# Optimization experiments

Measured on AMD Instinct MI355X. Metric: run time of the kernel, lower is better.

## Reference

```python
import jax, jax.numpy as jnp
import numpy as np

DIM = 96
HEADS = 4
HID = int(DIM * 2.66)  # 255, GDFN hidden width
B, H, W = 4, 128, 128


def _conv(x, w, b=None, groups=1):
    y = jax.lax.conv_general_dilated(x, w, (1, 1), 'SAME',
                                     dimension_numbers=('NCHW', 'OIHW', 'NCHW'),
                                     feature_group_count=groups)
    return y if b is None else y + b[None, :, None, None]


def _ln(x, w, b):
    # WithBias LayerNorm over channel dim (per pixel), biased variance, eps=1e-5
    mu = x.mean(1, keepdims=True)
    var = ((x - mu) ** 2).mean(1, keepdims=True)
    return (x - mu) / jnp.sqrt(var + 1e-5) * w[None, :, None, None] + b[None, :, None, None]


def _l2norm(x):
    # torch F.normalize(dim=-1): x / max(||x||_2, 1e-12)
    return x / jnp.maximum(jnp.linalg.norm(x, axis=-1, keepdims=True), 1e-12)


def _gelu(x):
    return jax.nn.gelu(x, approximate=False)


def setup_inputs() -> dict:
    key = jax.random.key(0)
    ks = iter(jax.random.split(key, 32))
    nrm = lambda shp, s=0.02: jax.random.normal(next(ks), shp, dtype=jnp.float32) * s
    d, h2 = DIM, HID
    inp = {
        'x': jax.random.normal(next(ks), (B, DIM, H, W), dtype=jnp.float32),
        # L_conv: 3x3(d->d,+b) GELU 1x1(d->1,+b)
        'Lc_w1': nrm((d, d, 3, 3)), 'Lc_b1': jnp.zeros((d,), jnp.float32),
        'Lc_w2': nrm((1, d, 1, 1)), 'Lc_b2': jnp.zeros((1,), jnp.float32),
        # R_conv: 3x3(d->d,+b) GELU 1x1(d->3,+b)
        'Rc_w1': nrm((d, d, 3, 3)), 'Rc_b1': jnp.zeros((d,), jnp.float32),
        'Rc_w2': nrm((3, d, 1, 1)), 'Rc_b2': jnp.zeros((3,), jnp.float32),
        # L_rein: 3x3(1->d,+b) GELU ; R_rein: 3x3(3->d,+b)
        'Lr_w': nrm((d, 1, 3, 3)), 'Lr_b': jnp.zeros((d,), jnp.float32),
        'Rr_w': nrm((d, 3, 3, 3)), 'Rr_b': jnp.zeros((d,), jnp.float32),
        # LayerNorms (WithBias)
        'n1_w': jnp.ones((d,), jnp.float32), 'n1_b': jnp.zeros((d,), jnp.float32),
        'nL_w': jnp.ones((d,), jnp.float32), 'nL_b': jnp.zeros((d,), jnp.float32),
        'n2_w': jnp.ones((d,), jnp.float32), 'n2_b': jnp.zeros((d,), jnp.float32),
        # Illum_Attention (bias=False)
        'temp': jnp.ones((HEADS, 1, 1), jnp.float32),
        'q_w': nrm((d, d, 1, 1)),
        'qd_w': nrm((d, d, 3, 3)),          # q_dwconv is a FULL 3x3 conv (no groups)
        'kv_w': nrm((2 * d, d, 1, 1)),
        'kvd_w': nrm((2 * d, 1, 3, 3)),     # depthwise, groups=2*dim
        'po_w': nrm((d, d, 1, 1)),
        # FeedForward (bias=False); NOTE: 'dwconv' here is a FULL 3x3 conv
        'pi_w': nrm((h2, d, 1, 1)),
        'fdw_w': nrm((h2, h2, 3, 3)),
        'fpo_w': nrm((d, h2, 1, 1)),
    }
    return inp


def reference(x, Lc_w1, Lc_b1, Lc_w2, Lc_b2, Rc_w1, Rc_b1, Rc_w2, Rc_b2,
              Lr_w, Lr_b, Rr_w, Rr_b, n1_w, n1_b, nL_w, nL_b, n2_w, n2_b,
              temp, q_w, qd_w, kv_w, kvd_w, po_w, pi_w, fdw_w, fpo_w):
    b, c, h, w = x.shape
    # Retinex decomposition heads
    L = _conv(_gelu(_conv(x, Lc_w1, Lc_b1)), Lc_w2, Lc_b2)   # [b,1,h,w]
    R = _conv(_gelu(_conv(x, Rc_w1, Rc_b1)), Rc_w2, Rc_b2)   # [b,3,h,w]
    L_rein = _gelu(_conv(jax.lax.stop_gradient(L), Lr_w, Lr_b))  # detach in torch
    R_rein = _conv(jax.lax.stop_gradient(R), Rr_w, Rr_b)
    # Illum_Guided_TransformerBlock: x = x + attn(norm1(x), normL(illum))
    xn = _ln(x, n1_w, n1_b)
    ill = _ln(L_rein, nL_w, nL_b)
    q = _conv(_conv(ill, q_w), qd_w)
    kv = _conv(_conv(xn, kv_w), kvd_w, groups=2 * c)
    k, v = jnp.split(kv, 2, axis=1)
    ch, hw = c // HEADS, h * w
    heads = lambda t: t.reshape(b, HEADS, ch, hw)
    qh, kh, vh = _l2norm(heads(q)), _l2norm(heads(k)), heads(v)
    # channel-wise attention: [b,heads,ch,ch]
    attn = jax.nn.softmax(jnp.einsum('bhci,bhdi->bhcd', qh, kh) * temp[None], axis=-1)
    out = jnp.einsum('bhcd,bhdi->bhci', attn, vh).reshape(b, c, h, w)
    x = x + _conv(out, po_w)
    # x = x + ffn(norm2(x))
    x2 = _ln(x, n2_w, n2_b)
    x = x + _conv(_gelu(_conv(_conv(x2, pi_w), fdw_w)), fpo_w)
    x = x + R_rein
    return (x, L, R)
```

## Files before the change

### kernel.cpp

```cpp
#include <hip/hip_runtime.h>

#define HWsz 16384
#define Wd 128

typedef unsigned short ushortT;
typedef unsigned int uintT;
typedef __attribute__((ext_vector_type(8))) short short8v;
typedef __attribute__((ext_vector_type(4))) float f32x4;
typedef __attribute__((ext_vector_type(16))) float f32x16;
typedef __attribute__((ext_vector_type(4))) unsigned short ushort4v;

__device__ __forceinline__ float gelu_f(float x){
    return 0.5f * x * (1.0f + erff(x * 0.70710678118654752f));
}
__device__ __forceinline__ ushortT f2b(float f){
    union { float f; uintT u; } v; v.f = f;
    uintT r = v.u + 0x7FFFu + ((v.u >> 16) & 1u);
    return (ushortT)(r >> 16);
}
__device__ __forceinline__ float b2f(ushortT u){
    union { uintT u; float f; } v; v.u = ((uintT)u) << 16; return v.f;
}
__device__ __forceinline__ void gload_lds16(const ushortT* g, ushortT* l){
    __builtin_amdgcn_global_load_lds(
        (const __attribute__((address_space(1))) void*)g,
        (__attribute__((address_space(3))) void*)l, 16, 0, 0);
}

__device__ __forceinline__ void pack3_one(int e, const float* __restrict__ w,
    ushortT* __restrict__ outp, int cout, int cin, int BN, int NCH)
{
    int j = e & 7; int r = e >> 3;
    int ocl = r % BN; r /= BN;
    int kg  = r & 3;  r >>= 2;
    int tap = r % 9;  r /= 9;
    int ch  = r % NCH;
    int nt  = r / NCH;
    int ci = ch*32 + kg*8 + j;
    int oc = nt*BN + ocl;
    float v = (oc < cout && ci < cin) ? w[((size_t)oc*cin + ci)*9 + tap] : 0.f;
    outp[e] = f2b(v);
}
__device__ __forceinline__ void pack1_one(int e, const float* __restrict__ w,
    ushortT* __restrict__ outp, int cout, int cin, int BN, int NCH)
{
    int j = e & 7; int r = e >> 3;
    int ocl = r % BN; r /= BN;
    int kg  = r & 3;  r >>= 2;
    int ch  = r % NCH;
    int nt  = r / NCH;
    int ci = ch*32 + kg*8 + j;
    int oc = nt*BN + ocl;
    float v = (oc < cout && ci < cin) ? w[(size_t)oc*cin + ci] : 0.f;
    outp[e] = f2b(v);
}
__global__ __launch_bounds__(256) void pack_all_kernel(
    const float* Lc, const float* Rc, const float* Qd, const float* Fd,
    const float* Q1, const float* KV1, const float* PI1, const float* FPO1,
    ushortT* dL, ushortT* dR, ushortT* dQ, ushortT* dF,
    ushortT* dq0, ushortT* dkv, ushortT* dpi, ushortT* dfpo)
{
    int e = blockIdx.x*256 + threadIdx.x;
    if      (e < 82944)  pack3_one(e,        Lc, dL, 96, 96, 48, 3);
    else if (e < 165888) pack3_one(e-82944,  Rc, dR, 96, 96, 48, 3);
    else if (e < 248832) pack3_one(e-165888, Qd, dQ, 96, 96, 48, 3);
    else if (e < 912384) pack3_one(e-248832, Fd, dF, 255,255, 48, 8);
    else if (e < 921600) pack1_one(e-912384, Q1, dq0, 96, 96, 96, 3);
    else if (e < 940032) pack1_one(e-921600, KV1,dkv, 192,96, 48, 3);
    else if (e < 964608) pack1_one(e-940032, PI1,dpi, 255,96, 64, 3);
    else if (e < 989184) pack1_one(e-964608, FPO1,dfpo,96,255, 96, 8);
}

__global__ __launch_bounds__(256) void tonhwc_ln_kernel(
    const float* __restrict__ in, const float* __restrict__ w,
    const float* __restrict__ bias, ushortT* __restrict__ xh,
    ushortT* __restrict__ xnh)
{
    const int p = blockIdx.x*256 + threadIdx.x;
    const int b = blockIdx.y;
    const float* ip = in + (size_t)b*96*HWsz + p;
    float v[96]; float s=0.f;
#pragma unroll
    for(int c=0;c<96;c++){ v[c]=ip[(size_t)c*HWsz]; s+=v[c]; }
    const float mu = s*(1.f/96.f);
    float s2=0.f;
#pragma unroll
    for(int c=0;c<96;c++){ float d=v[c]-mu; s2+=d*d; }
    const float inv = 1.f/sqrtf(s2*(1.f/96.f)+1e-5f);
    ushortT* op1 = xh  + ((size_t)b*HWsz + p)*96;
    ushortT* op2 = xnh + ((size_t)b*HWsz + p)*96;
#pragma unroll
    for (int g=0; g<12; g++){
        uint4 pk1, pk2; uintT a4[4], n4[4];
#pragma unroll
        for (int i=0;i<4;i++){
            float x0 = v[g*8+2*i], x1v = v[g*8+2*i+1];
            a4[i] = (uintT)f2b(x0) | ((uintT)f2b(x1v)<<16);
            float r0 = (x0-mu)*inv*w[g*8+2*i]+bias[g*8+2*i];
            float r1 = (x1v-mu)*inv*w[g*8+2*i+1]+bias[g*8+2*i+1];
            n4[i] = (uintT)f2b(r0) | ((uintT)f2b(r1)<<16);
        }
        pk1.x=a4[0]; pk1.y=a4[1]; pk1.z=a4[2]; pk1.w=a4[3];
        pk2.x=n4[0]; pk2.y=n4[1]; pk2.z=n4[2]; pk2.w=n4[3];
        *(uint4*)(op1 + g*8) = pk1;
        *(uint4*)(op2 + g*8) = pk2;
    }
}

template<int NG, int NCH, int ACT, int TWOOUT, int OMODE>
__global__ __launch_bounds__(256,3) void conv3x3_v4(
    const ushortT* __restrict__ inh,
    const ushortT* __restrict__ wpk1, const ushortT* __restrict__ wpk2,
    const float* __restrict__ bias1, const float* __restrict__ bias2,
    ushortT* __restrict__ out1, ushortT* __restrict__ out2,
    int cout, int ocpad)
{
    constexpr int BN = NG*16;
    constexpr int Cpad = NCH*32;
    constexpr int WCH4 = 9*4*BN;
    constexpr int WI = (WCH4 + 255)/256;
    __shared__ __align__(16) ushortT As[4*324*8];
    __shared__ __align__(16) ushortT Ws[WCH4*8];

    const int tid = threadIdx.x;
    const int l   = tid & 63;
    const int wv  = tid >> 6;
    const int l15 = l & 15;
    const int kg  = l >> 4;
    const int tix = blockIdx.x & 7, tiy = blockIdx.x >> 3;
    const int b   = blockIdx.z;
    const int x0 = tix*16, y0 = tiy*16;

    int nt = blockIdx.y;
    const ushortT* wpk; const float* bias; ushortT* outp; int ntw;
    if (TWOOUT && nt >= 2){ wpk = wpk2; bias = bias2; outp = out2; ntw = nt-2; }
    else { wpk = wpk1; bias = bias1; outp = out1; ntw = nt; }
    const int ocbase = ntw*BN;

    f32x4 acc[4][NG];
#pragma unroll
    for (int m=0;m<4;m++)
#pragma unroll
        for (int n=0;n<NG;n++) acc[m][n] = (f32x4){0.f,0.f,0.f,0.f};

    const ushortT* inb = inh + (size_t)b*HWsz*Cpad;

    for (int ch=0; ch<NCH; ch++){
        __syncthreads();
        for (int t=tid; t<1296; t+=256){
            int p = t>>2, g = t&3;
            int hy = p/18, hx = p - hy*18;
            int gy = y0 + hy - 1, gx = x0 + hx - 1;
            uint4 v; v.x=0u; v.y=0u; v.z=0u; v.w=0u;
            if ((unsigned)gy < 128u && (unsigned)gx < 128u)
                v = *(const uint4*)(inb + (size_t)(gy*Wd+gx)*Cpad + ch*32 + g*8);
            *(uint4*)(As + (g*324+p)*8) = v;
        }
        {
            const ushortT* wsrc = wpk + ((size_t)ntw*NCH + ch)*(WCH4*8);
#pragma unroll
            for (int i=0; i<WI; i++){
                int t = i*256 + tid;
                if ((WCH4 & 255) == 0 || t < WCH4)
                    gload_lds16(wsrc + (size_t)t*8, Ws + (size_t)t*8);
            }
        }
        __syncthreads();
#pragma unroll
        for (int tp=0; tp<9; tp++){
            const int dy = tp/3, dx = tp - dy*3;
            short8v bf[NG];
#pragma unroll
            for (int n=0;n<NG;n++)
                bf[n] = *(const short8v*)(Ws + ((size_t)(tp*4 + kg)*BN + n*16 + l15)*8);
#pragma unroll
            for (int mg=0;mg<4;mg++){
                short8v a = *(const short8v*)(As + (kg*324 + (wv*4+mg+dy)*18 + l15+dx)*8);
#pragma unroll
                for (int n=0;n<NG;n++)
                    acc[mg][n] = __builtin_amdgcn_mfma_f32_16x16x32_bf16(a, bf[n], acc[mg][n], 0,0,0);
            }
        }
    }
    if (OMODE == 1){
        __syncthreads();
        ushortT* Ts = As + wv*1024;
#pragma unroll
        for (int mg=0;mg<4;mg++){
            int gy = y0 + wv*4 + mg;
            ushortT* orow = outp + ((size_t)b*HWsz + gy*Wd + x0)*ocpad + ocbase;
#pragma unroll
            for (int n=0;n<NG;n++){
                int ocl = n*16 + l15;
                int oc  = ocbase + ocl;
                float bs = (bias && oc < cout) ? bias[oc] : 0.f;
#pragma unroll
                for (int j=0;j<4;j++){
                    int pxj = kg*4 + j;
                    float r = 0.f;
                    if (oc < cout){ r = acc[mg][n][j] + bs; if (ACT) r = gelu_f(r); }
                    int seg = ((ocl>>3) + pxj) & 7;
                    Ts[pxj*64 + seg*8 + (ocl&7)] = f2b(r);
                }
            }
#pragma unroll
            for (int ps=0; ps < (BN+31)/32; ps++){
                int rpx = l & 15;
                int rs  = (l>>4) + ps*4;
                if (rs*8 < BN && ocbase + rs*8 + 8 <= ocpad){
                    int pseg = (rs + rpx) & 7;
                    short8v v = *(const short8v*)(Ts + rpx*64 + pseg*8);
                    *(short8v*)(orow + (size_t)rpx*ocpad + rs*8) = v;
                }
            }
        }
    } else {
#pragma unroll
        for (int n=0;n<NG;n++){
            int oc = ocbase + n*16 + l15;
            if (oc < cout){
                float bs = bias ? bias[oc] : 0.f;
#pragma unroll
                for (int mg=0;mg<4;mg++){
                    int gy = y0 + wv*4 + mg;
                    int gx = x0 + kg*4;
                    ushort4v pk;
#pragma unroll
                    for (int j=0;j<4;j++){
                        float r = acc[mg][n][j] + bs;
                        if (ACT) r = gelu_f(r);
                        pk[j] = f2b(r);
                    }
                    *(ushort4v*)(outp + ((size_t)b*cout + oc)*HWsz + gy*Wd + gx) = pk;
                }
            }
        }
    }
}

template<int NGW, int NCH>
__global__ __launch_bounds__(256) void gemm1x1_v2(
    const ushortT* __restrict__ inh, const ushortT* __restrict__ wpk,
    ushortT* __restrict__ outp, int cout, int ocpad)
{
    constexpr int BN = NGW*16;
    constexpr int Cpad = NCH*32;
    __shared__ __align__(16) ushortT Ts[4*16*64];

    const int tid = threadIdx.x;
    const int l = tid & 63, wv = tid >> 6, l15 = l & 15, kg = l >> 4;
    const int p0 = blockIdx.x*64;
    const int b  = blockIdx.z;
    const int nt = wv, ocbase = wv*BN;
    const ushortT* inb = inh + (size_t)b*HWsz*Cpad;

    f32x4 acc[4][NGW];
#pragma unroll
    for (int m=0;m<4;m++)
#pragma unroll
        for (int n=0;n<NGW;n++) acc[m][n] = (f32x4){0.f,0.f,0.f,0.f};

#pragma unroll
    for (int ch=0; ch<NCH; ch++){
        short8v a[4], bw[NGW];
#pragma unroll
        for (int mg=0; mg<4; mg++)
            a[mg] = *(const short8v*)(inb + (size_t)(p0 + mg*16 + l15)*Cpad + ch*32 + kg*8);
#pragma unroll
        for (int n=0;n<NGW;n++)
            bw[n] = *(const short8v*)(wpk + (((size_t)(nt*NCH + ch)*4 + kg)*BN + n*16 + l15)*8);
#pragma unroll
        for (int mg=0;mg<4;mg++)
#pragma unroll
            for (int n=0;n<NGW;n++)
                acc[mg][n] = __builtin_amdgcn_mfma_f32_16x16x32_bf16(a[mg], bw[n], acc[mg][n], 0,0,0);
    }
    ushortT* Tw = Ts + wv*1024;
#pragma unroll
    for (int mg=0;mg<4;mg++){
        ushortT* orow = outp + ((size_t)b*HWsz + p0 + mg*16)*ocpad + ocbase;
#pragma unroll
        for (int n=0;n<NGW;n++){
            int ocl = n*16 + l15;
            int oc  = ocbase + ocl;
#pragma unroll
            for (int j=0;j<4;j++){
                int pxj = kg*4 + j;
                float r = (oc < cout) ? acc[mg][n][j] : 0.f;
                int seg = ((ocl>>3) + pxj) & 7;
                Tw[pxj*64 + seg*8 + (ocl&7)] = f2b(r);
            }
        }
#pragma unroll
        for (int ps=0; ps < (BN+31)/32; ps++){
            int rpx = l & 15;
            int rs  = (l>>4) + ps*4;
            if (rs*8 < BN){
                int pseg = (rs + rpx) & 7;
                short8v v = *(const short8v*)(Tw + rpx*64 + pseg*8);
                *(short8v*)(orow + (size_t)rpx*ocpad + rs*8) = v;
            }
        }
    }
}

template<int NG, int NCH, int RES, int OMODE, int XMAP>
__global__ __launch_bounds__(256) void gemm1x1_mfma(
    const ushortT* __restrict__ inh, const ushortT* __restrict__ wpk, int wstride_z,
    const float* __restrict__ res1, const ushortT* __restrict__ res2b,
    void* __restrict__ outv, int cout, int ocpad)
{
    constexpr int BN = NG*16;
    constexpr int Cpad = NCH*32;
    constexpr int LSTR = (BN <= 64) ? 64 : 128;
    constexpr int MASK = LSTR/8 - 1;
    __shared__ __align__(16) ushortT TsS[(OMODE==1) ? 4*16*LSTR : 16];

    const int tid = threadIdx.x;
    const int l = tid & 63, wv = tid >> 6, l15 = l & 15, kg = l >> 4;
    int chunk = blockIdx.x, nt = blockIdx.y, b = blockIdx.z;
    const int p0 = chunk*256 + wv*64;
    const ushortT* inb = inh + (size_t)b*HWsz*Cpad;
    const ushortT* wp  = wpk + (size_t)b*wstride_z;

    f32x4 acc[4][NG];
#pragma unroll
    for (int m=0;m<4;m++)
#pragma unroll
        for (int n=0;n<NG;n++) acc[m][n] = (f32x4){0.f,0.f,0.f,0.f};

#pragma unroll
    for (int ch=0; ch<NCH; ch++){
        short8v a[4], bw[NG];
#pragma unroll
        for (int mg=0; mg<4; mg++)
            a[mg] = *(const short8v*)(inb + (size_t)(p0 + mg*16 + l15)*Cpad + ch*32 + kg*8);
#pragma unroll
        for (int n=0;n<NG;n++)
            bw[n] = *(const short8v*)(wp + (((size_t)(nt*NCH + ch)*4 + kg)*BN + n*16 + l15)*8);
#pragma unroll
        for (int mg=0;mg<4;mg++)
#pragma unroll
            for (int n=0;n<NG;n++)
                acc[mg][n] = __builtin_amdgcn_mfma_f32_16x16x32_bf16(a[mg], bw[n], acc[mg][n], 0,0,0);
    }
    if (OMODE == 0){
        float* out = (float*)outv;
#pragma unroll
        for (int n=0;n<NG;n++){
            int oc = nt*BN + n*16 + l15;
            if (oc < cout){
#pragma unroll
                for (int mg=0;mg<4;mg++){
                    int pix = p0 + mg*16 + kg*4;
                    size_t idx = ((size_t)b*cout + oc)*HWsz + pix;
                    float4 r;
                    r.x = acc[mg][n][0]; r.y = acc[mg][n][1];
                    r.z = acc[mg][n][2]; r.w = acc[mg][n][3];
                    if (RES>=1){ float4 q = *(const float4*)(res1+idx); r.x+=q.x;r.y+=q.y;r.z+=q.z;r.w+=q.w; }
                    if (RES>=2){
                        ushort4v q = *(const ushort4v*)(res2b+idx);
                        r.x+=b2f(q[0]); r.y+=b2f(q[1]); r.z+=b2f(q[2]); r.w+=b2f(q[3]);
                    }
                    *(float4*)(out + idx) = r;
                }
            }
        }
    } else {
        ushortT* outp = (ushortT*)outv;
        ushortT* Ts = TsS + wv*(16*LSTR);
#pragma unroll
        for (int mg=0;mg<4;mg++){
            ushortT* orow = outp + ((size_t)b*HWsz + p0 + mg*16)*ocpad + nt*BN;
#pragma unroll
            for (int n=0;n<NG;n++){
                int ocl = n*16 + l15;
                int oc  = nt*BN + ocl;
#pragma unroll
                for (int j=0;j<4;j++){
                    int pxj = kg*4 + j;
                    float r = (oc < cout) ? acc[mg][n][j] : 0.f;
                    int seg = ((ocl>>3) + pxj) & MASK;
                    Ts[pxj*LSTR + seg*8 + (ocl&7)] = f2b(r);
                }
            }
#pragma unroll
            for (int ps=0; ps < (BN+31)/32; ps++){
                int rpx = l & 15;
                int rs  = (l>>4) + ps*4;
                if (rs*8 < BN){
                    int pseg = (rs + rpx) & MASK;
                    short8v v = *(const short8v*)(Ts + rpx*LSTR + pseg*8);
                    *(short8v*)(orow + (size_t)rpx*ocpad + rs*8) = v;
                }
            }
        }
    }
}

__global__ __launch_bounds__(256) void pvpo_ln_kernel(
    const ushortT* __restrict__ vh, const ushortT* __restrict__ Mpk,
    const float* __restrict__ xres, const float* __restrict__ lnw,
    const float* __restrict__ lnb, float* __restrict__ x1out,
    ushortT* __restrict__ x2nh)
{
    constexpr int BN = 96, NG = 6, NCH = 3, Cpad = 96, LSTR = 128, MASK = 15;
    __shared__ __align__(16) ushortT TsS[4*16*LSTR];

    const int tid = threadIdx.x;
    const int l = tid & 63, wv = tid >> 6, l15 = l & 15, kg = l >> 4;
    const int b = blockIdx.z;
    const int p0 = blockIdx.x*256 + wv*64;
    const ushortT* inb = vh + (size_t)b*HWsz*Cpad;
    const ushortT* wp  = Mpk + (size_t)b*9216;

    f32x4 acc[4][NG];
#pragma unroll
    for (int m=0;m<4;m++)
#pragma unroll
        for (int n=0;n<NG;n++) acc[m][n] = (f32x4){0.f,0.f,0.f,0.f};

#pragma unroll
    for (int ch=0; ch<NCH; ch++){
        short8v a[4], bw[NG];
#pragma unroll
        for (int mg=0; mg<4; mg++)
            a[mg] = *(const short8v*)(inb + (size_t)(p0 + mg*16 + l15)*Cpad + ch*32 + kg*8);
#pragma unroll
        for (int n=0;n<NG;n++)
            bw[n] = *(const short8v*)(wp + (((size_t)ch*4 + kg)*BN + n*16 + l15)*8);
#pragma unroll
        for (int mg=0;mg<4;mg++)
#pragma unroll
            for (int n=0;n<NG;n++)
                acc[mg][n] = __builtin_amdgcn_mfma_f32_16x16x32_bf16(a[mg], bw[n], acc[mg][n], 0,0,0);
    }
#pragma unroll
    for (int mg=0;mg<4;mg++){
#pragma unroll
        for (int n=0;n<NG;n++){
            int oc = n*16 + l15;
            int pix = p0 + mg*16 + kg*4;
            size_t idx = ((size_t)b*96 + oc)*HWsz + pix;
            float4 q = *(const float4*)(xres+idx);
            acc[mg][n][0] += q.x; acc[mg][n][1] += q.y;
            acc[mg][n][2] += q.z; acc[mg][n][3] += q.w;
            float4 r;
            r.x = acc[mg][n][0]; r.y = acc[mg][n][1];
            r.z = acc[mg][n][2]; r.w = acc[mg][n][3];
            *(float4*)(x1out + idx) = r;
        }
    }
    float nv[4][NG][4];
#pragma unroll
    for (int mg=0;mg<4;mg++){
#pragma unroll
        for (int j=0;j<4;j++){
            float s = 0.f;
#pragma unroll
            for (int n=0;n<NG;n++) s += acc[mg][n][j];
#pragma unroll
            for (int m=1; m<16; m<<=1) s += __shfl_xor(s, m, 64);
            float mu = s*(1.f/96.f);
            float s2 = 0.f;
#pragma unroll
            for (int n=0;n<NG;n++){ float d = acc[mg][n][j]-mu; s2 += d*d; }
#pragma unroll
            for (int m=1; m<16; m<<=1) s2 += __shfl_xor(s2, m, 64);
            float inv = 1.f/sqrtf(s2*(1.f/96.f) + 1e-5f);
#pragma unroll
            for (int n=0;n<NG;n++){
                int oc = n*16 + l15;
                nv[mg][n][j] = (acc[mg][n][j]-mu)*inv*lnw[oc]+lnb[oc];
            }
        }
    }
    ushortT* Ts = TsS + wv*(16*LSTR);
#pragma unroll
    for (int mg=0;mg<4;mg++){
        ushortT* orow = x2nh + ((size_t)b*HWsz + p0 + mg*16)*96;
#pragma unroll
        for (int n=0;n<NG;n++){
            int ocl = n*16 + l15;
#pragma unroll
            for (int j=0;j<4;j++){
                int pxj = kg*4 + j;
                int seg = ((ocl>>3) + pxj) & MASK;
                Ts[pxj*LSTR + seg*8 + (ocl&7)] = f2b(nv[mg][n][j]);
            }
        }
#pragma unroll
        for (int ps=0; ps<3; ps++){
            int rpx = l & 15;
            int rs  = (l>>4) + ps*4;
            int pseg = (rs + rpx) & MASK;
            short8v v = *(const short8v*)(Ts + rpx*LSTR + pseg*8);
            *(short8v*)(orow + (size_t)rpx*96 + rs*8) = v;
        }
    }
}

template<int NOUT>
__global__ __launch_bounds__(256) void head1x1_kernel(
    const ushortT* __restrict__ inh, const float* __restrict__ w,
    const float* __restrict__ bias, float* __restrict__ out)
{
    __shared__ float lw[NOUT*96];
    const int tid = threadIdx.x;
    for (int t=tid; t<NOUT*96; t+=256) lw[t] = w[t];
    __syncthreads();
    const int p = blockIdx.x*256 + tid;
    const int b = blockIdx.y;
    const ushortT* ip = inh + ((size_t)b*HWsz + p)*96;
    float v[96];
#pragma unroll
    for (int g=0; g<12; g++){
        short8v s = *(const short8v*)(ip + g*8);
#pragma unroll
        for (int i=0;i<8;i++) v[g*8+i] = b2f((ushortT)s[i]);
    }
#pragma unroll
    for (int oc=0; oc<NOUT; oc++){
        float acc = bias[oc];
#pragma unroll
        for (int c=0;c<96;c++) acc += v[c]*lw[oc*96+c];
        out[((size_t)b*NOUT + oc)*HWsz + p] = acc;
    }
}

__global__ __launch_bounds__(256) void lrein_ln_kernel(
    const float* __restrict__ L, const float* __restrict__ w,
    const float* __restrict__ bias, const float* __restrict__ lnw,
    const float* __restrict__ lnb, ushortT* __restrict__ outh)
{
    __shared__ float sw[864], sb[96], sn1[96], sn2[96];
    const int tid = threadIdx.x;
    for (int t=tid; t<864; t+=256) sw[t] = w[t];
    if (tid < 96){ sb[tid]=bias[tid]; sn1[tid]=lnw[tid]; sn2[tid]=lnb[tid]; }
    __syncthreads();
    const int p = blockIdx.x*256 + tid;
    const int b = blockIdx.y;
    const int y = p>>7, x = p&127;
    const float* ib = L + (size_t)b*HWsz;
    float win[9];
#pragma unroll
    for (int dy=0;dy<3;dy++)
#pragma unroll
        for (int dx=0;dx<3;dx++){
            int gy=y+dy-1, gx=x+dx-1;
            win[dy*3+dx] = ((unsigned)gy<128u && (unsigned)gx<128u) ? ib[gy*Wd+gx] : 0.f;
        }
    float v[96]; float s=0.f;
#pragma unroll
    for (int c=0;c<96;c++){
        float a = sb[c];
#pragma unroll
        for (int t=0;t<9;t++) a += win[t]*sw[c*9+t];
        a = gelu_f(a);
        v[c]=a; s+=a;
    }
    const float mu = s*(1.f/96.f);
    float s2=0.f;
#pragma unroll
    for (int c=0;c<96;c++){ float d=v[c]-mu; s2+=d*d; }
    const float inv = 1.f/sqrtf(s2*(1.f/96.f)+1e-5f);
    ushortT* op = outh + ((size_t)b*HWsz + p)*96;
#pragma unroll
    for (int g=0; g<12; g++){
        uint4 pk; uintT w4[4];
#pragma unroll
        for (int i=0;i<4;i++){
            float r0 = (v[g*8+2*i]-mu)*inv*sn1[g*8+2*i]+sn2[g*8+2*i];
            float r1 = (v[g*8+2*i+1]-mu)*inv*sn1[g*8+2*i+1]+sn2[g*8+2*i+1];
            w4[i] = (uintT)f2b(r0) | ((uintT)f2b(r1)<<16);
        }
        pk.x=w4[0]; pk.y=w4[1]; pk.z=w4[2]; pk.w=w4[3];
        *(uint4*)(op + g*8) = pk;
    }
}

__global__ __launch_bounds__(256) void conv3x3_rr_kernel(
    const float* __restrict__ in, const float* __restrict__ w,
    const float* __restrict__ bias, ushortT* __restrict__ out)
{
    __shared__ float sw[216], sb[8];
    const int oc0 = blockIdx.y*8;
    if (threadIdx.x < 216) sw[threadIdx.x] = w[(size_t)oc0*27 + threadIdx.x];
    if (threadIdx.x < 8)   sb[threadIdx.x] = bias[oc0 + threadIdx.x];
    __syncthreads();
    const int p = blockIdx.x*256+threadIdx.x;
    const int b = blockIdx.z;
    const int y=p>>7, x=p&127;
    const float* ib = in + (size_t)b*3*HWsz;
    float win[27];
#pragma unroll
    for (int ci=0;ci<3;ci++)
#pragma unroll
        for (int dy=0;dy<3;dy++)
#pragma unroll
            for (int dx=0;dx<3;dx++){
                int gy=y+dy-1, gx=x+dx-1;
                win[ci*9+dy*3+dx] = ((unsigned)gy<128u && (unsigned)gx<128u)
                    ? ib[(size_t)ci*HWsz + gy*Wd+gx] : 0.f;
            }
#pragma unroll
    for (int i=0;i<8;i++){
        float acc = sb[i];
#pragma unroll
        for (int t=0;t<27;t++) acc += win[t]*sw[i*27+t];
        out[((size_t)b*96 + oc0+i)*HWsz + p] = f2b(acc);
    }
}

__global__ __launch_bounds__(256) void dw_nhwc_kernel(
    const ushortT* __restrict__ inh, const float* __restrict__ w,
    ushortT* __restrict__ kout, ushortT* __restrict__ vouth)
{
    const int p = blockIdx.x*256+threadIdx.x;
    const int c0 = blockIdx.y*8;
    const int b = blockIdx.z;
    const int y=p>>7, x=p&127;
    float lw[72];
#pragma unroll
    for (int i=0;i<8;i++)
#pragma unroll
        for (int t=0;t<9;t++) lw[i*9+t] = w[(size_t)(c0+i)*9 + t];
    const ushortT* ib = inh + (size_t)b*HWsz*192;
    float acc[8];
#pragma unroll
    for (int i=0;i<8;i++) acc[i]=0.f;
#pragma unroll
    for(int dy=0;dy<3;dy++){
        int gy=y+dy-1;
        if((unsigned)gy<128u){
#pragma unroll
            for(int dx=0;dx<3;dx++){
                int gx=x+dx-1;
                if((unsigned)gx<128u){
                    short8v s = *(const short8v*)(ib + (size_t)(gy*Wd+gx)*192 + c0);
#pragma unroll
                    for (int i=0;i<8;i++) acc[i] += b2f((ushortT)s[i])*lw[i*9+dy*3+dx];
                }
            }
        }
    }
    if (c0 < 96){
#pragma unroll
        for (int i=0;i<8;i++)
            kout[((size_t)b*96 + c0+i)*HWsz + p] = f2b(acc[i]);
    } else {
        ushortT* op = vouth + ((size_t)b*HWsz + p)*96 + (c0-96);
        uint4 pk;
        pk.x = (uintT)f2b(acc[0]) | ((uintT)f2b(acc[1])<<16);
        pk.y = (uintT)f2b(acc[2]) | ((uintT)f2b(acc[3])<<16);
        pk.z = (uintT)f2b(acc[4]) | ((uintT)f2b(acc[5])<<16);
        pk.w = (uintT)f2b(acc[6]) | ((uintT)f2b(acc[7])<<16);
        *(uint4*)op = pk;
    }
}

__global__ __launch_bounds__(256) void rownorm_bf16_kernel(
    const ushortT* __restrict__ qb, const ushortT* __restrict__ kb,
    float* __restrict__ invqk)
{
    __shared__ float red[256];
    const int r = blockIdx.x;
    const ushortT* ip = (r < 384) ? (qb + (size_t)r*HWsz) : (kb + (size_t)(r-384)*HWsz);
    float s=0.f;
    const ushortT* tp = ip + threadIdx.x*64;
#pragma unroll
    for (int g=0; g<8; g++){
        short8v v = *(const short8v*)(tp + g*8);
#pragma unroll
        for (int i=0;i<8;i++){ float f = b2f((ushortT)v[i]); s += f*f; }
    }
    red[threadIdx.x]=s; __syncthreads();
    for(int st=128; st>0; st>>=1){
        if(threadIdx.x<st) red[threadIdx.x]+=red[threadIdx.x+st];
        __syncthreads();
    }
    if(threadIdx.x==0) invqk[r] = 1.f/fmaxf(sqrtf(red[0]), 1e-12f);
}

__global__ __launch_bounds__(256) void qk_mfma_kernel(
    const ushortT* __restrict__ qb, const ushortT* __restrict__ kb,
    float* __restrict__ part)
{
    const int tid = threadIdx.x;
    const int l = tid & 63, wv = tid >> 6;
    const int chunk = blockIdx.x*4 + wv;
    const int bh = blockIdx.y, b = bh>>2, h = bh&3;
    const int ch = min(l & 31, 23);
    const int kh = (l >> 5)*8;
    const ushortT* qp = qb + ((size_t)b*96 + h*24 + ch)*HWsz + chunk*512 + kh;
    const ushortT* kp = kb + ((size_t)b*96 + h*24 + ch)*HWsz + chunk*512 + kh;
    f32x16 acc;
#pragma unroll
    for (int r=0;r<16;r++) acc[r]=0.f;
    for (int ks=0; ks<32; ks++){
        short8v a  = *(const short8v*)(qp + ks*16);
        short8v bb = *(const short8v*)(kp + ks*16);
        acc = __builtin_amdgcn_mfma_f32_32x32x16_bf16(a, bb, acc, 0,0,0);
    }
    float* op = part + ((size_t)chunk*16 + bh)*1024;
    const int col = l & 31;
#pragma unroll
    for (int r=0;r<16;r++){
        int row = (r&3) + 8*(r>>2) + 4*(l>>5);
        op[row*32 + col] = acc[r];
    }
}

__global__ __launch_bounds__(576) void softmax_kernel(
    const float* __restrict__ part, const float* __restrict__ invq,
    const float* __restrict__ invk, const float* __restrict__ temp,
    float* __restrict__ attn)
{
    __shared__ float l[576];
    const int bh=blockIdx.x, b=bh>>2, h=bh&3;
    const int tid=threadIdx.x;
    const int i=tid/24, j=tid-i*24;
    float s=0.f;
    for (int c=0;c<32;c++) s += part[((size_t)c*16 + bh)*1024 + i*32 + j];
    l[tid] = s * invq[b*96+h*24+i] * invk[b*96+h*24+j] * temp[h];
    __syncthreads();
    if(tid<24){
        float m=-1e30f;
#pragma unroll
        for(int jj=0;jj<24;jj++) m = fmaxf(m, l[tid*24+jj]);
        float e[24]; float sm=0.f;
#pragma unroll
        for(int jj=0;jj<24;jj++){ e[jj]=__expf(l[tid*24+jj]-m); sm+=e[jj]; }
        float isv = 1.f/sm;
#pragma unroll
        for(int jj=0;jj<24;jj++) attn[(size_t)bh*576 + tid*24 + jj] = e[jj]*isv;
    }
}

__global__ __launch_bounds__(256) void mkM_kernel(
    const float* __restrict__ attn, const float* __restrict__ po_w,
    ushortT* __restrict__ Mpk)
{
    const int b = blockIdx.x;
    for (int e = threadIdx.x; e < 9216; e += 256){
        int oc = e / 96, d = e - oc*96;
        int h = d / 24, dl = d - h*24;
        const float* aw = attn + ((size_t)(b*4+h))*576 + dl;
        const float* pw = po_w + (size_t)oc*96 + h*24;
        float s = 0.f;
#pragma unroll
        for (int c=0;c<24;c++) s += pw[c]*aw[c*24];
        int ch = d>>5, kg = (d>>3)&3, j = d&7;
        Mpk[(size_t)b*9216 + ((size_t)(ch*4+kg)*96 + oc)*8 + j] = f2b(s);
    }
}

extern "C" void kernel_launch(void* const* d_in, const int* in_sizes, int n_in,
                              void* d_out, int out_size, void* d_ws, size_t ws_size,
                              hipStream_t stream)
{
    const float* x     = (const float*)d_in[0];
    const float* Lc_w1 = (const float*)d_in[1];
    const float* Lc_b1 = (const float*)d_in[2];
    const float* Lc_w2 = (const float*)d_in[3];
    const float* Lc_b2 = (const float*)d_in[4];
    const float* Rc_w1 = (const float*)d_in[5];
    const float* Rc_b1 = (const float*)d_in[6];
    const float* Rc_w2 = (const float*)d_in[7];
    const float* Rc_b2 = (const float*)d_in[8];
    const float* Lr_w  = (const float*)d_in[9];
    const float* Lr_b  = (const float*)d_in[10];
    const float* Rr_w  = (const float*)d_in[11];
    const float* Rr_b  = (const float*)d_in[12];
    const float* n1_w  = (const float*)d_in[13];
    const float* n1_b  = (const float*)d_in[14];
    const float* nL_w  = (const float*)d_in[15];
    const float* nL_b  = (const float*)d_in[16];
    const float* n2_w  = (const float*)d_in[17];
    const float* n2_b  = (const float*)d_in[18];
    const float* temp  = (const float*)d_in[19];
    const float* q_w   = (const float*)d_in[20];
    const float* qd_w  = (const float*)d_in[21];
    const float* kv_w  = (const float*)d_in[22];
    const float* kvd_w = (const float*)d_in[23];
    const float* po_w  = (const float*)d_in[24];
    const float* pi_w  = (const float*)d_in[25];
    const float* fdw_w = (const float*)d_in[26];
    const float* fpo_w = (const float*)d_in[27];

    char* base = (char*)d_ws;
    ushortT* xh   = (ushortT*)(base + 0);
    ushortT* f0h  = (ushortT*)(base + 0);
    ushortT* Lh   = (ushortT*)(base + 33554432);
    ushortT* kv0h = (ushortT*)(base + 33554432);
    ushortT* f1h  = (ushortT*)(base + 33554432);
    ushortT* Rh   = (ushortT*)(base + 67108864);
    ushortT* vh   = (ushortT*)(base + 67108864);
    ushortT* x2nh = (ushortT*)(base + 67108864);
    ushortT* illh = (ushortT*)(base + 79691776);
    ushortT* xnh  = (ushortT*)(base + 92274688);
    ushortT* q0h  = (ushortT*)(base + 104857600);
    ushortT* qb   = (ushortT*)(base + 117440512);
    float*   x1   = (float*)(base + 117440512);
    ushortT* kb   = (ushortT*)(base + 142606336);
    ushortT* Bb   = (ushortT*)(base + 155189248);
    char* smb = base + 167772160;
    ushortT* wpkL = (ushortT*)smb;   smb += 165888;
    ushortT* wpkR = (ushortT*)smb;   smb += 165888;
    ushortT* wpkQ = (ushortT*)smb;   smb += 165888;
    ushortT* wpkF = (ushortT*)smb;   smb += 1327104;
    ushortT* wq0  = (ushortT*)smb;   smb += 18432;
    ushortT* wkv  = (ushortT*)smb;   smb += 36864;
    ushortT* wpi  = (ushortT*)smb;   smb += 49152;
    ushortT* wfpo = (ushortT*)smb;   smb += 49152;
    ushortT* Mpk  = (ushortT*)smb;   smb += 73728;
    float* invqk  = (float*)smb;     smb += 3072;
    float* part   = (float*)smb;     smb += 2097152;
    float* attn   = (float*)smb;     smb += 36864;

    float* out_x = (float*)d_out;
    float* out_L = out_x + (size_t)4*96*HWsz;
    float* out_R = out_L + (size_t)4*HWsz;

    dim3 blk(256);

    hipLaunchKernelGGL(pack_all_kernel, dim3(3864), blk, 0, stream,
        Lc_w1, Rc_w1, qd_w, fdw_w, q_w, kv_w, pi_w, fpo_w,
        wpkL, wpkR, wpkQ, wpkF, wq0, wkv, wpi, wfpo);
    hipLaunchKernelGGL(tonhwc_ln_kernel, dim3(64,4), blk, 0, stream, x, n1_w, n1_b, xh, xnh);

    hipLaunchKernelGGL((conv3x3_v4<3,3,1,1,1>), dim3(64,4,4), blk, 0, stream,
        xh, wpkL, wpkR, Lc_b1, Rc_b1, Lh, Rh, 96, 96);
    hipLaunchKernelGGL((head1x1_kernel<1>), dim3(64,4), blk, 0, stream, Lh, Lc_w2, Lc_b2, out_L);
    hipLaunchKernelGGL((head1x1_kernel<3>), dim3(64,4), blk, 0, stream, Rh, Rc_w2, Rc_b2, out_R);
    hipLaunchKernelGGL(lrein_ln_kernel, dim3(64,4), blk, 0, stream, out_L, Lr_w, Lr_b, nL_w, nL_b, illh);
    hipLaunchKernelGGL(conv3x3_rr_kernel, dim3(64,12,4), blk, 0, stream, out_R, Rr_w, Rr_b, Bb);

    hipLaunchKernelGGL((gemm1x1_mfma<6,3,0,1,0>), dim3(64,1,4), blk, 0, stream,
        illh, wq0, 0, nullptr, nullptr, (void*)q0h, 96, 96);
    hipLaunchKernelGGL((conv3x3_v4<3,3,0,0,2>), dim3(64,2,4), blk, 0, stream,
        q0h, wpkQ, wpkQ, nullptr, nullptr, qb, qb, 96, 0);
    hipLaunchKernelGGL((gemm1x1_v2<3,3>), dim3(256,1,4), blk, 0, stream,
        xnh, wkv, kv0h, 192, 192);
    hipLaunchKernelGGL(dw_nhwc_kernel, dim3(64,24,4), blk, 0, stream, kv0h, kvd_w, kb, vh);

    hipLaunchKernelGGL(rownorm_bf16_kernel, dim3(768), blk, 0, stream, qb, kb, invqk);
    hipLaunchKernelGGL(qk_mfma_kernel, dim3(8,16), blk, 0, stream, qb, kb, part);
    hipLaunchKernelGGL(softmax_kernel, dim3(16), dim3(576), 0, stream, part, invqk, invqk+384, temp, attn);
    hipLaunchKernelGGL(mkM_kernel, dim3(4), blk, 0, stream, attn, po_w, Mpk);
    hipLaunchKernelGGL(pvpo_ln_kernel, dim3(64,1,4), blk, 0, stream,
        vh, Mpk, x, n2_w, n2_b, x1, x2nh);

    hipLaunchKernelGGL((gemm1x1_v2<4,3>), dim3(256,1,4), blk, 0, stream,
        x2nh, wpi, f0h, 255, 256);
    hipLaunchKernelGGL((conv3x3_v4<3,8,1,0,1>), dim3(64,6,4), blk, 0, stream,
        f0h, wpkF, wpkF, nullptr, nullptr, f1h, f1h, 255, 256);
    hipLaunchKernelGGL((gemm1x1_mfma<6,8,2,0,0>), dim3(64,1,4), blk, 0, stream,
        f1h, wfpo, 0, x1, Bb, (void*)out_x, 96, 0);
}
```

Measured before the change: 359.4 us.

## Merge small head/attention kernels and store the x1 residual in bf16

Merges the L and R 1x1 head kernels into one launch, the L-rein and R-rein convolutions into one launch, row-norm with the QK MFMA, and softmax with the attention/projection matrix build. Launch count drops and small kernels run concurrently inside a single grid. The intermediate residual x1 is now written as bf16 instead of fp32 and added back in bf16 in the final GEMM epilogue. This halves that tensor's traffic but lowers the precision of the residual path.

```diff
diff --git a/kernel.cpp b/kernel.cpp
--- a/kernel.cpp
+++ b/kernel.cpp
@@ -357,10 +357,12 @@
                     float4 r;
                     r.x = acc[mg][n][0]; r.y = acc[mg][n][1];
                     r.z = acc[mg][n][2]; r.w = acc[mg][n][3];
-                    if (RES>=1){ float4 q = *(const float4*)(res1+idx); r.x+=q.x;r.y+=q.y;r.z+=q.z;r.w+=q.w; }
-                    if (RES>=2){
-                        ushort4v q = *(const ushort4v*)(res2b+idx);
-                        r.x+=b2f(q[0]); r.y+=b2f(q[1]); r.z+=b2f(q[2]); r.w+=b2f(q[3]);
+                    if (RES==3){
+                        const ushortT* r1b = (const ushortT*)res1;
+                        ushort4v q1 = *(const ushort4v*)(r1b+idx);
+                        r.x+=b2f(q1[0]); r.y+=b2f(q1[1]); r.z+=b2f(q1[2]); r.w+=b2f(q1[3]);
+                        ushort4v q2 = *(const ushort4v*)(res2b+idx);
+                        r.x+=b2f(q2[0]); r.y+=b2f(q2[1]); r.z+=b2f(q2[2]); r.w+=b2f(q2[3]);
                     }
                     *(float4*)(out + idx) = r;
                 }
@@ -401,7 +403,7 @@
 __global__ __launch_bounds__(256) void pvpo_ln_kernel(
     const ushortT* __restrict__ vh, const ushortT* __restrict__ Mpk,
     const float* __restrict__ xres, const float* __restrict__ lnw,
-    const float* __restrict__ lnb, float* __restrict__ x1out,
+    const float* __restrict__ lnb, ushortT* __restrict__ x1b,
     ushortT* __restrict__ x2nh)
 {
     constexpr int BN = 96, NG = 6, NCH = 3, Cpad = 96, LSTR = 128, MASK = 15;
@@ -445,10 +447,10 @@
             float4 q = *(const float4*)(xres+idx);
             acc[mg][n][0] += q.x; acc[mg][n][1] += q.y;
             acc[mg][n][2] += q.z; acc[mg][n][3] += q.w;
-            float4 r;
-            r.x = acc[mg][n][0]; r.y = acc[mg][n][1];
-            r.z = acc[mg][n][2]; r.w = acc[mg][n][3];
-            *(float4*)(x1out + idx) = r;
+            ushort4v pk;
+            pk[0]=f2b(acc[mg][n][0]); pk[1]=f2b(acc[mg][n][1]);
+            pk[2]=f2b(acc[mg][n][2]); pk[3]=f2b(acc[mg][n][3]);
+            *(ushort4v*)(x1b + idx) = pk;
         }
     }
     float nv[4][NG][4];
@@ -500,14 +502,22 @@
     }
 }
 
-template<int NOUT>
-__global__ __launch_bounds__(256) void head1x1_kernel(
-    const ushortT* __restrict__ inh, const float* __restrict__ w,
-    const float* __restrict__ bias, float* __restrict__ out)
-{
-    __shared__ float lw[NOUT*96];
+__global__ __launch_bounds__(256) void headLR_kernel(
+    const ushortT* __restrict__ Lh, const ushortT* __restrict__ Rh,
+    const float* __restrict__ wL, const float* __restrict__ bL,
+    const float* __restrict__ wR, const float* __restrict__ bR,
+    float* __restrict__ outL, float* __restrict__ outR)
+{
+    __shared__ float lw[288], lb[3];
+    const int sel = blockIdx.z;
+    const int NOUT = sel ? 3 : 1;
+    const ushortT* inh = sel ? Rh : Lh;
+    const float* w = sel ? wR : wL;
+    const float* bias = sel ? bR : bL;
+    float* out = sel ? outR : outL;
     const int tid = threadIdx.x;
     for (int t=tid; t<NOUT*96; t+=256) lw[t] = w[t];
+    if (tid < NOUT) lb[tid] = bias[tid];
     __syncthreads();
     const int p = blockIdx.x*256 + tid;
     const int b = blockIdx.y;
@@ -520,95 +530,94 @@
         for (int i=0;i<8;i++) v[g*8+i] = b2f((ushortT)s[i]);
     }
 #pragma unroll
-    for (int oc=0; oc<NOUT; oc++){
-        float acc = bias[oc];
-#pragma unroll
-        for (int c=0;c<96;c++) acc += v[c]*lw[oc*96+c];
-        out[((size_t)b*NOUT + oc)*HWsz + p] = acc;
-    }
-}
-
-__global__ __launch_bounds__(256) void lrein_ln_kernel(
-    const float* __restrict__ L, const float* __restrict__ w,
-    const float* __restrict__ bias, const float* __restrict__ lnw,
-    const float* __restrict__ lnb, ushortT* __restrict__ outh)
+    for (int oc=0; oc<3; oc++){
+        if (oc < NOUT){
+            float acc = lb[oc];
+#pragma unroll
+            for (int c=0;c<96;c++) acc += v[c]*lw[oc*96+c];
+            out[((size_t)b*NOUT + oc)*HWsz + p] = acc;
+        }
+    }
+}
+
+__global__ __launch_bounds__(256) void lrein_rr_kernel(
+    const float* __restrict__ L, const float* __restrict__ Lrw,
+    const float* __restrict__ Lrb, const float* __restrict__ lnw,
+    const float* __restrict__ lnb, ushortT* __restrict__ illh,
+    const float* __restrict__ R, const float* __restrict__ Rrw,
+    const float* __restrict__ Rrb, ushortT* __restrict__ Bb)
 {
     __shared__ float sw[864], sb[96], sn1[96], sn2[96];
     const int tid = threadIdx.x;
-    for (int t=tid; t<864; t+=256) sw[t] = w[t];
-    if (tid < 96){ sb[tid]=bias[tid]; sn1[tid]=lnw[tid]; sn2[tid]=lnb[tid]; }
-    __syncthreads();
-    const int p = blockIdx.x*256 + tid;
-    const int b = blockIdx.y;
-    const int y = p>>7, x = p&127;
-    const float* ib = L + (size_t)b*HWsz;
-    float win[9];
-#pragma unroll
-    for (int dy=0;dy<3;dy++)
-#pragma unroll
-        for (int dx=0;dx<3;dx++){
-            int gy=y+dy-1, gx=x+dx-1;
-            win[dy*3+dx] = ((unsigned)gy<128u && (unsigned)gx<128u) ? ib[gy*Wd+gx] : 0.f;
-        }
-    float v[96]; float s=0.f;
-#pragma unroll
-    for (int c=0;c<96;c++){
-        float a = sb[c];
-#pragma unroll
-        for (int t=0;t<9;t++) a += win[t]*sw[c*9+t];
-        a = gelu_f(a);
-        v[c]=a; s+=a;
-    }
-    const float mu = s*(1.f/96.f);
-    float s2=0.f;
-#pragma unroll
-    for (int c=0;c<96;c++){ float d=v[c]-mu; s2+=d*d; }
-    const float inv = 1.f/sqrtf(s2*(1.f/96.f)+1e-5f);
-    ushortT* op = outh + ((size_t)b*HWsz + p)*96;
-#pragma unroll
-    for (int g=0; g<12; g++){
-        uint4 pk; uintT w4[4];
-#pragma unroll
-        for (int i=0;i<4;i++){
-            float r0 = (v[g*8+2*i]-mu)*inv*sn1[g*8+2*i]+sn2[g*8+2*i];
-            float r1 = (v[g*8+2*i+1]-mu)*inv*sn1[g*8+2*i+1]+sn2[g*8+2*i+1];
-            w4[i] = (uintT)f2b(r0) | ((uintT)f2b(r1)<<16);
-        }
-        pk.x=w4[0]; pk.y=w4[1]; pk.z=w4[2]; pk.w=w4[3];
-        *(uint4*)(op + g*8) = pk;
-    }
-}
-
-__global__ __launch_bounds__(256) void conv3x3_rr_kernel(
-    const float* __restrict__ in, const float* __restrict__ w,
-    const float* __restrict__ bias, ushortT* __restrict__ out)
-{
-    __shared__ float sw[216], sb[8];
-    const int oc0 = blockIdx.y*8;
-    if (threadIdx.x < 216) sw[threadIdx.x] = w[(size_t)oc0*27 + threadIdx.x];
-    if (threadIdx.x < 8)   sb[threadIdx.x] = bias[oc0 + threadIdx.x];
-    __syncthreads();
-    const int p = blockIdx.x*256+threadIdx.x;
     const int b = blockIdx.z;
-    const int y=p>>7, x=p&127;
-    const float* ib = in + (size_t)b*3*HWsz;
-    float win[27];
-#pragma unroll
-    for (int ci=0;ci<3;ci++)
+    if (blockIdx.y == 12){
+        for (int t=tid; t<864; t+=256) sw[t] = Lrw[t];
+        if (tid < 96){ sb[tid]=Lrb[tid]; sn1[tid]=lnw[tid]; sn2[tid]=lnb[tid]; }
+        __syncthreads();
+        const int p = blockIdx.x*256 + tid;
+        const int y = p>>7, x = p&127;
+        const float* ib = L + (size_t)b*HWsz;
+        float win[9];
 #pragma unroll
         for (int dy=0;dy<3;dy++)
 #pragma unroll
             for (int dx=0;dx<3;dx++){
                 int gy=y+dy-1, gx=x+dx-1;
-                win[ci*9+dy*3+dx] = ((unsigned)gy<128u && (unsigned)gx<128u)
-                    ? ib[(size_t)ci*HWsz + gy*Wd+gx] : 0.f;
-            }
-#pragma unroll
-    for (int i=0;i<8;i++){
-        float acc = sb[i];
-#pragma unroll
-        for (int t=0;t<27;t++) acc += win[t]*sw[i*27+t];
-        out[((size_t)b*96 + oc0+i)*HWsz + p] = f2b(acc);
+                win[dy*3+dx] = ((unsigned)gy<128u && (unsigned)gx<128u) ? ib[gy*Wd+gx] : 0.f;
+            }
+        float v[96]; float s=0.f;
+#pragma unroll
+        for (int c=0;c<96;c++){
+            float a = sb[c];
+#pragma unroll
+            for (int t=0;t<9;t++) a += win[t]*sw[c*9+t];
+            a = gelu_f(a);
+            v[c]=a; s+=a;
+        }
+        const float mu = s*(1.f/96.f);
+        float s2=0.f;
+#pragma unroll
+        for (int c=0;c<96;c++){ float d=v[c]-mu; s2+=d*d; }
+        const float inv = 1.f/sqrtf(s2*(1.f/96.f)+1e-5f);
+        ushortT* op = illh + ((size_t)b*HWsz + p)*96;
+#pragma unroll
+        for (int g=0; g<12; g++){
+            uint4 pk; uintT w4[4];
+#pragma unroll
+            for (int i=0;i<4;i++){
+                float r0 = (v[g*8+2*i]-mu)*inv*sn1[g*8+2*i]+sn2[g*8+2*i];
+                float r1 = (v[g*8+2*i+1]-mu)*inv*sn1[g*8+2*i+1]+sn2[g*8+2*i+1];
+                w4[i] = (uintT)f2b(r0) | ((uintT)f2b(r1)<<16);
+            }
+            pk.x=w4[0]; pk.y=w4[1]; pk.z=w4[2]; pk.w=w4[3];
+            *(uint4*)(op + g*8) = pk;
+        }
+    } else {
+        const int oc0 = blockIdx.y*8;
+        if (tid < 216) sw[tid] = Rrw[(size_t)oc0*27 + tid];
+        if (tid < 8)   sb[tid] = Rrb[oc0 + tid];
+        __syncthreads();
+        const int p = blockIdx.x*256 + tid;
+        const int y=p>>7, x=p&127;
+        const float* ib = R + (size_t)b*3*HWsz;
+        float win[27];
+#pragma unroll
+        for (int ci=0;ci<3;ci++)
+#pragma unroll
+            for (int dy=0;dy<3;dy++)
+#pragma unroll
+                for (int dx=0;dx<3;dx++){
+                    int gy=y+dy-1, gx=x+dx-1;
+                    win[ci*9+dy*3+dx] = ((unsigned)gy<128u && (unsigned)gx<128u)
+                        ? ib[(size_t)ci*HWsz + gy*Wd+gx] : 0.f;
+                }
+#pragma unroll
+        for (int i=0;i<8;i++){
+            float acc = sb[i];
+#pragma unroll
+            for (int t=0;t<27;t++) acc += win[t]*sw[i*27+t];
+            Bb[((size_t)b*96 + oc0+i)*HWsz + p] = f2b(acc);
+        }
     }
 }
 
@@ -659,99 +668,98 @@
     }
 }
 
-__global__ __launch_bounds__(256) void rownorm_bf16_kernel(
+__global__ __launch_bounds__(256) void qk_rn_kernel(
     const ushortT* __restrict__ qb, const ushortT* __restrict__ kb,
-    float* __restrict__ invqk)
-{
-    __shared__ float red[256];
-    const int r = blockIdx.x;
-    const ushortT* ip = (r < 384) ? (qb + (size_t)r*HWsz) : (kb + (size_t)(r-384)*HWsz);
-    float s=0.f;
-    const ushortT* tp = ip + threadIdx.x*64;
-#pragma unroll
-    for (int g=0; g<8; g++){
-        short8v v = *(const short8v*)(tp + g*8);
-#pragma unroll
-        for (int i=0;i<8;i++){ float f = b2f((ushortT)v[i]); s += f*f; }
-    }
-    red[threadIdx.x]=s; __syncthreads();
-    for(int st=128; st>0; st>>=1){
-        if(threadIdx.x<st) red[threadIdx.x]+=red[threadIdx.x+st];
-        __syncthreads();
-    }
-    if(threadIdx.x==0) invqk[r] = 1.f/fmaxf(sqrtf(red[0]), 1e-12f);
-}
-
-__global__ __launch_bounds__(256) void qk_mfma_kernel(
-    const ushortT* __restrict__ qb, const ushortT* __restrict__ kb,
-    float* __restrict__ part)
-{
+    float* __restrict__ part, float* __restrict__ invqk)
+{
+    const int i = blockIdx.x;
     const int tid = threadIdx.x;
-    const int l = tid & 63, wv = tid >> 6;
-    const int chunk = blockIdx.x*4 + wv;
-    const int bh = blockIdx.y, b = bh>>2, h = bh&3;
-    const int ch = min(l & 31, 23);
-    const int kh = (l >> 5)*8;
-    const ushortT* qp = qb + ((size_t)b*96 + h*24 + ch)*HWsz + chunk*512 + kh;
-    const ushortT* kp = kb + ((size_t)b*96 + h*24 + ch)*HWsz + chunk*512 + kh;
-    f32x16 acc;
-#pragma unroll
-    for (int r=0;r<16;r++) acc[r]=0.f;
-    for (int ks=0; ks<32; ks++){
-        short8v a  = *(const short8v*)(qp + ks*16);
-        short8v bb = *(const short8v*)(kp + ks*16);
-        acc = __builtin_amdgcn_mfma_f32_32x32x16_bf16(a, bb, acc, 0,0,0);
-    }
-    float* op = part + ((size_t)chunk*16 + bh)*1024;
-    const int col = l & 31;
-#pragma unroll
-    for (int r=0;r<16;r++){
-        int row = (r&3) + 8*(r>>2) + 4*(l>>5);
-        op[row*32 + col] = acc[r];
-    }
-}
-
-__global__ __launch_bounds__(576) void softmax_kernel(
+    if (i < 128){
+        const int l = tid & 63, wv = tid >> 6;
+        const int bh = i & 15, c4 = i >> 4;
+        const int chunk = c4*4 + wv;
+        const int b = bh>>2, h = bh&3;
+        const int ch = min(l & 31, 23);
+        const int kh = (l >> 5)*8;
+        const ushortT* qp = qb + ((size_t)b*96 + h*24 + ch)*HWsz + chunk*512 + kh;
+        const ushortT* kp = kb + ((size_t)b*96 + h*24 + ch)*HWsz + chunk*512 + kh;
+        f32x16 acc;
+#pragma unroll
+        for (int r=0;r<16;r++) acc[r]=0.f;
+        for (int ks=0; ks<32; ks++){
+            short8v a  = *(const short8v*)(qp + ks*16);
+            short8v bb = *(const short8v*)(kp + ks*16);
+            acc = __builtin_amdgcn_mfma_f32_32x32x16_bf16(a, bb, acc, 0,0,0);
+        }
+        float* op = part + ((size_t)chunk*16 + bh)*1024;
+        const int col = l & 31;
+#pragma unroll
+        for (int r=0;r<16;r++){
+            int row = (r&3) + 8*(r>>2) + 4*(l>>5);
+            op[row*32 + col] = acc[r];
+        }
+    } else {
+        __shared__ float red[256];
+        const int r = i - 128;
+        const ushortT* ip = (r < 384) ? (qb + (size_t)r*HWsz) : (kb + (size_t)(r-384)*HWsz);
+        float s=0.f;
+        const ushortT* tp = ip + tid*64;
+#pragma unroll
+        for (int g=0; g<8; g++){
+            short8v v = *(const short8v*)(tp + g*8);
+#pragma unroll
+            for (int k=0;k<8;k++){ float f = b2f((ushortT)v[k]); s += f*f; }
+        }
+        red[tid]=s; __syncthreads();
+        for(int st=128; st>0; st>>=1){
+            if(tid<st) red[tid]+=red[tid+st];
+            __syncthreads();
+        }
+        if(tid==0) invqk[r] = 1.f/fmaxf(sqrtf(red[0]), 1e-12f);
+    }
+}
+
+__global__ __launch_bounds__(576) void softmax_mkM_kernel(
     const float* __restrict__ part, const float* __restrict__ invq,
     const float* __restrict__ invk, const float* __restrict__ temp,
-    float* __restrict__ attn)
-{
-    __shared__ float l[576];
-    const int bh=blockIdx.x, b=bh>>2, h=bh&3;
-    const int tid=threadIdx.x;
-    const int i=tid/24, j=tid-i*24;
-    float s=0.f;
-    for (int c=0;c<32;c++) s += part[((size_t)c*16 + bh)*1024 + i*32 + j];
-    l[tid] = s * invq[b*96+h*24+i] * invk[b*96+h*24+j] * temp[h];
+    const float* __restrict__ po_w, ushortT* __restrict__ Mpk)
+{
+    __shared__ float attnS[4][576];
+    const int b = blockIdx.x;
+    const int tid = threadIdx.x;
+    const int i = tid/24, j = tid - i*24;
+#pragma unroll
+    for (int h=0; h<4; h++){
+        int bh = b*4 + h;
+        float s = 0.f;
+        for (int c=0;c<32;c++) s += part[((size_t)c*16 + bh)*1024 + i*32 + j];
+        attnS[h][tid] = s * invq[b*96+h*24+i] * invk[b*96+h*24+j] * temp[h];
+    }
     __syncthreads();
-    if(tid<24){
-        float m=-1e30f;
-#pragma unroll
-        for(int jj=0;jj<24;jj++) m = fmaxf(m, l[tid*24+jj]);
+    if (tid < 96){
+        int h = tid/24, r = tid - h*24;
+        float* row = &attnS[h][r*24];
+        float m = -1e30f;
+#pragma unroll
+        for (int jj=0;jj<24;jj++) m = fmaxf(m, row[jj]);
         float e[24]; float sm=0.f;
 #pragma unroll
-        for(int jj=0;jj<24;jj++){ e[jj]=__expf(l[tid*24+jj]-m); sm+=e[jj]; }
+        for (int jj=0;jj<24;jj++){ e[jj]=__expf(row[jj]-m); sm+=e[jj]; }
         float isv = 1.f/sm;
 #pragma unroll
-        for(int jj=0;jj<24;jj++) attn[(size_t)bh*576 + tid*24 + jj] = e[jj]*isv;
-    }
-}
-
-__global__ __launch_bounds__(256) void mkM_kernel(
-    const float* __restrict__ attn, const float* __restrict__ po_w,
-    ushortT* __restrict__ Mpk)
-{
-    const int b = blockIdx.x;
-    for (int e = threadIdx.x; e < 9216; e += 256){
-        int oc = e / 96, d = e - oc*96;
+        for (int jj=0;jj<24;jj++) row[jj] = e[jj]*isv;
+    }
+    __syncthreads();
+    for (int e1 = tid; e1 < 9216; e1 += 576){
+        int oc = e1 / 96, d = e1 - oc*96;
         int h = d / 24, dl = d - h*24;
-        const float* aw = attn + ((size_t)(b*4+h))*576 + dl;
+        const float* aw = &attnS[h][dl];
         const float* pw = po_w + (size_t)oc*96 + h*24;
         float s = 0.f;
 #pragma unroll
         for (int c=0;c<24;c++) s += pw[c]*aw[c*24];
-        int ch = d>>5, kg = (d>>3)&3, j = d&7;
-        Mpk[(size_t)b*9216 + ((size_t)(ch*4+kg)*96 + oc)*8 + j] = f2b(s);
+        int ch = d>>5, kg = (d>>3)&3, jx = d&7;
+        Mpk[(size_t)b*9216 + ((size_t)(ch*4+kg)*96 + oc)*8 + jx] = f2b(s);
     }
 }
 
@@ -801,7 +809,7 @@
     ushortT* xnh  = (ushortT*)(base + 92274688);
     ushortT* q0h  = (ushortT*)(base + 104857600);
     ushortT* qb   = (ushortT*)(base + 117440512);
-    float*   x1   = (float*)(base + 117440512);
+    ushortT* x1b  = (ushortT*)(base + 117440512);
     ushortT* kb   = (ushortT*)(base + 142606336);
     ushortT* Bb   = (ushortT*)(base + 155189248);
     char* smb = base + 167772160;
@@ -816,7 +824,6 @@
     ushortT* Mpk  = (ushortT*)smb;   smb += 73728;
     float* invqk  = (float*)smb;     smb += 3072;
     float* part   = (float*)smb;     smb += 2097152;
-    float* attn   = (float*)smb;     smb += 36864;
 
     float* out_x = (float*)d_out;
     float* out_L = out_x + (size_t)4*96*HWsz;
@@ -831,10 +838,10 @@
 
     hipLaunchKernelGGL((conv3x3_v4<3,3,1,1,1>), dim3(64,4,4), blk, 0, stream,
         xh, wpkL, wpkR, Lc_b1, Rc_b1, Lh, Rh, 96, 96);
-    hipLaunchKernelGGL((head1x1_kernel<1>), dim3(64,4), blk, 0, stream, Lh, Lc_w2, Lc_b2, out_L);
-    hipLaunchKernelGGL((head1x1_kernel<3>), dim3(64,4), blk, 0, stream, Rh, Rc_w2, Rc_b2, out_R);
-    hipLaunchKernelGGL(lrein_ln_kernel, dim3(64,4), blk, 0, stream, out_L, Lr_w, Lr_b, nL_w, nL_b, illh);
-    hipLaunchKernelGGL(conv3x3_rr_kernel, dim3(64,12,4), blk, 0, stream, out_R, Rr_w, Rr_b, Bb);
+    hipLaunchKernelGGL(headLR_kernel, dim3(64,4,2), blk, 0, stream,
+        Lh, Rh, Lc_w2, Lc_b2, Rc_w2, Rc_b2, out_L, out_R);
+    hipLaunchKernelGGL(lrein_rr_kernel, dim3(64,13,4), blk, 0, stream,
+        out_L, Lr_w, Lr_b, nL_w, nL_b, illh, out_R, Rr_w, Rr_b, Bb);
 
     hipLaunchKernelGGL((gemm1x1_mfma<6,3,0,1,0>), dim3(64,1,4), blk, 0, stream,
         illh, wq0, 0, nullptr, nullptr, (void*)q0h, 96, 96);
@@ -844,17 +851,16 @@
         xnh, wkv, kv0h, 192, 192);
     hipLaunchKernelGGL(dw_nhwc_kernel, dim3(64,24,4), blk, 0, stream, kv0h, kvd_w, kb, vh);
 
-    hipLaunchKernelGGL(rownorm_bf16_kernel, dim3(768), blk, 0, stream, qb, kb, invqk);
-    hipLaunchKernelGGL(qk_mfma_kernel, dim3(8,16), blk, 0, stream, qb, kb, part);
-    hipLaunchKernelGGL(softmax_kernel, dim3(16), dim3(576), 0, stream, part, invqk, invqk+384, temp, attn);
-    hipLaunchKernelGGL(mkM_kernel, dim3(4), blk, 0, stream, attn, po_w, Mpk);
+    hipLaunchKernelGGL(qk_rn_kernel, dim3(896), blk, 0, stream, qb, kb, part, invqk);
+    hipLaunchKernelGGL(softmax_mkM_kernel, dim3(4), dim3(576), 0, stream,
+        part, invqk, invqk+384, temp, po_w, Mpk);
     hipLaunchKernelGGL(pvpo_ln_kernel, dim3(64,1,4), blk, 0, stream,
-        vh, Mpk, x, n2_w, n2_b, x1, x2nh);
+        vh, Mpk, x, n2_w, n2_b, x1b, x2nh);
 
     hipLaunchKernelGGL((gemm1x1_v2<4,3>), dim3(256,1,4), blk, 0, stream,
         x2nh, wpi, f0h, 255, 256);
     hipLaunchKernelGGL((conv3x3_v4<3,8,1,0,1>), dim3(64,6,4), blk, 0, stream,
         f0h, wpkF, wpkF, nullptr, nullptr, f1h, f1h, 255, 256);
-    hipLaunchKernelGGL((gemm1x1_mfma<6,8,2,0,0>), dim3(64,1,4), blk, 0, stream,
-        f1h, wfpo, 0, x1, Bb, (void*)out_x, 96, 0);
-}
+    hipLaunchKernelGGL((gemm1x1_mfma<6,8,3,0,0>), dim3(64,1,4), blk, 0, stream,
+        f1h, wfpo, 0, (const float*)x1b, Bb, (void*)out_x, 96, 0);
+}
```

Measured after the change: 373.1 us. +3.8%, slower.
